# Kernel optimization log

Hardware: AMD Instinct MI355X
Metric: run time of the kernel (lower is better)

## Reference

```python
import jax, jax.numpy as jnp
import numpy as np

P = 3; Q = 3                 # spline degrees (deg_p, deg_q)
OUT_U = 64; OUT_V = 64       # surface evaluation grid
W_CTRL = 1.0; W_SURF = 1.0
B = 1024; MU_MAX = 32; MV_MAX = 32
EPS = 1e-5                   # SurfEval samples u,v in [eps, 1-eps]


def _open_uniform_knots(n_valid, degree, n_max):
    """Clamped open-uniform knot vector for n_valid ctrl pts, padded to static
    length n_max+degree+1. Entries beyond the valid span are clamped to 1.0,
    which makes the padded basis functions identically zero on [eps, 1-eps]."""
    L = n_valid + degree + 1  # true (ragged) knot count, traced int
    k = jnp.arange(n_max + degree + 1)
    interior = k.astype(jnp.float32) / (L - 1).astype(jnp.float32)
    return jnp.where(k <= degree, 0.0, jnp.where(k >= L - 1 - degree, 1.0, interior))


def _bspline_basis(kv, degree, u):
    """Cox-de Boor, vectorized over u. kv: (n_max+degree+1,), u: (U,).
    Returns (U, n_max) basis matrix; padded columns are exactly zero."""
    N = ((u[None, :] >= kv[:-1, None]) & (u[None, :] < kv[1:, None])).astype(jnp.float32)
    for d in range(1, degree + 1):
        m = N.shape[0] - 1  # number of basis funcs at this level
        den1 = kv[d:d + m] - kv[:m]
        den2 = kv[d + 1:d + 1 + m] - kv[1:1 + m]
        s1 = jnp.where((den1 > 0)[:, None],
                       (u[None, :] - kv[:m, None]) / jnp.where(den1 > 0, den1, 1.0)[:, None], 0.0)
        s2 = jnp.where((den2 > 0)[:, None],
                       (kv[d + 1:d + 1 + m, None] - u[None, :]) / jnp.where(den2 > 0, den2, 1.0)[:, None], 0.0)
        N = s1 * N[:m] + s2 * N[1:m + 1]
    return N.T  # (U, n_max)


def _eval_surface(ctrl, mask_b, u, v):
    """NURBS surface eval for one sample with ragged (Mu_i, Mv_i) via padded
    knots/basis; unit weights => rational division by basis partition sum."""
    mu = jnp.maximum(jnp.sum(jnp.any(mask_b > 0, axis=1)), P + 1)
    mv = jnp.maximum(jnp.sum(jnp.any(mask_b > 0, axis=0)), Q + 1)
    Bu = _bspline_basis(_open_uniform_knots(mu, P, MU_MAX), P, u)  # (OUT_U, MU_MAX)
    Bv = _bspline_basis(_open_uniform_knots(mv, Q, MV_MAX), Q, v)  # (OUT_V, MV_MAX)
    num = jnp.einsum('ui,vj,ijd->uvd', Bu, Bv, ctrl)               # (OUT_U, OUT_V, 3)
    den = Bu.sum(-1)[:, None] * Bv.sum(-1)[None, :]                # unit-weight denom
    return num / den[..., None]


def setup_inputs() -> dict:
    key = jax.random.key(0)
    k1, k2, k3, k4, k5 = jax.random.split(key, 5)
    # ragged true control sizes per sample, >= degree+1
    mu = jax.random.randint(k1, (B,), P + 1, MU_MAX + 1)
    mv = jax.random.randint(k2, (B,), Q + 1, MV_MAX + 1)
    mask = ((jnp.arange(MU_MAX)[None, :, None] < mu[:, None, None]) &
            (jnp.arange(MV_MAX)[None, None, :] < mv[:, None, None])).astype(jnp.float32)
    ctrl_pred_pad = jax.random.normal(k3, (B, MU_MAX, MV_MAX, 3), jnp.float32)
    ctrl_gt_pad = jax.random.normal(k4, (B, MU_MAX, MV_MAX, 3), jnp.float32)
    xyz_samples = jax.random.normal(k5, (B, OUT_U, OUT_V, 3), jnp.float32)
    return {"ctrl_pred_pad": ctrl_pred_pad, "ctrl_gt_pad": ctrl_gt_pad,
            "mask": mask, "xyz_samples": xyz_samples}


def reference(ctrl_pred_pad, ctrl_gt_pad, mask, xyz_samples):
    # masked control-point MSE
    diff2 = ((ctrl_pred_pad - ctrl_gt_pad) ** 2).sum(-1)
    loss_ctrl = (diff2 * mask).sum() / jnp.maximum(mask.sum() * 3.0, 1.0)
    # batched ragged surface evaluation
    u = jnp.linspace(EPS, 1.0 - EPS, OUT_U)
    v = jnp.linspace(EPS, 1.0 - EPS, OUT_V)
    surf = jax.vmap(lambda c, m: _eval_surface(c, m, u, v))(ctrl_pred_pad, mask)
    loss_surf = jnp.mean((surf.reshape(B, -1, 3) - xyz_samples.reshape(B, -1, 3)) ** 2)
    total = W_CTRL * loss_ctrl + W_SURF * loss_surf  # original computes total BEFORE nan-guard
    bad = jnp.isnan(surf).any() | jnp.isinf(surf).any()
    surf_mse = jnp.where(bad, jnp.float32(1e6), loss_surf)
    return total, loss_ctrl, surf_mse
```

## Files before the change

### kernel.cpp

```cpp
#include <hip/hip_runtime.h>
#include <math.h>

#define MU_MAXC 32
#define MV_MAXC 32
#define OUT_UC  64
#define OUT_VC  64
#define DEG     3
#define NKNOT   (MU_MAXC + DEG + 1)
#define EPSV    1e-5f

__global__ void zero_ws_kernel(double* acc, int* bad) {
    acc[0] = 0.0; acc[1] = 0.0; acc[2] = 0.0; bad[0] = 0;
}

template <int MODE>
__launch_bounds__(256)
__global__ void nurbs_loss_kernel(const float* __restrict__ ctrl_pred,
                                  const float* __restrict__ ctrl_gt,
                                  const float* __restrict__ mask,
                                  const float* __restrict__ xyz,
                                  double* __restrict__ pd, int Bcnt,
                                  int* __restrict__ badp)
{
    const int b   = blockIdx.x;
    const int tid = threadIdx.x;

    __shared__ float s_tmp[OUT_UC * MV_MAXC * 3];
    __shared__ float s_mask[1024];
    __shared__ float s_Bu4[4 * OUT_UC];
    __shared__ float s_Bv4[4 * OUT_VC];
    __shared__ int   s_uoff[OUT_UC];
    __shared__ int   s_voff[OUT_VC];
    __shared__ float s_invSumBu[OUT_UC];
    __shared__ float s_knots_u[NKNOT];
    __shared__ float s_knots_v[NKNOT];
    __shared__ int   s_rowany[MU_MAXC];
    __shared__ int   s_colany[MV_MAXC];
    __shared__ int   s_mu, s_mv, s_bad;
    __shared__ float s_wred[4], s_wred2[4];
    __shared__ float s_ctrl_diff, s_ctrl_mask;

    if (tid < 32) { s_rowany[tid] = 0; s_colany[tid] = 0; }
    if (tid == 0) s_bad = 0;
    __syncthreads();

    float lsum_mask = 0.f;
    #pragma unroll
    for (int k = 0; k < 4; k++) {
        const int cell = tid + 256 * k;
        const float m  = mask[b * 1024 + cell];
        s_mask[cell] = m;
        lsum_mask += m;
        if (m > 0.f) { s_rowany[cell >> 5] = 1; s_colany[cell & 31] = 1; }
    }
    __syncthreads();

    float lsum_diff = 0.f;
    {
        const float4* p4 = (const float4*)(ctrl_pred + (size_t)b * 3072);
        const float4* g4 = (const float4*)(ctrl_gt   + (size_t)b * 3072);
        #pragma unroll
        for (int k = 0; k < 3; k++) {
            const int e4 = tid + 256 * k;
            const float4 p = p4[e4];
            const float4 g = g4[e4];
            const int e = e4 * 4;
            const float dx = p.x - g.x, dy = p.y - g.y, dz = p.z - g.z, dw = p.w - g.w;
            lsum_diff += s_mask[(e + 0) / 3] * dx * dx
                       + s_mask[(e + 1) / 3] * dy * dy
                       + s_mask[(e + 2) / 3] * dz * dz
                       + s_mask[(e + 3) / 3] * dw * dw;
        }
    }
    #pragma unroll
    for (int off = 32; off > 0; off >>= 1) {
        lsum_mask += __shfl_down(lsum_mask, off);
        lsum_diff += __shfl_down(lsum_diff, off);
    }
    if ((tid & 63) == 0) { s_wred[tid >> 6] = lsum_mask; s_wred2[tid >> 6] = lsum_diff; }
    __syncthreads();

    if (tid == 0) {
        int cu = 0, cv = 0;
        #pragma unroll
        for (int i = 0; i < 32; i++) { cu += s_rowany[i]; cv += s_colany[i]; }
        s_mu = cu > (DEG + 1) ? cu : (DEG + 1);
        s_mv = cv > (DEG + 1) ? cv : (DEG + 1);
        s_ctrl_mask = s_wred[0] + s_wred[1] + s_wred[2] + s_wred[3];
        s_ctrl_diff = s_wred2[0] + s_wred2[1] + s_wred2[2] + s_wred2[3];
    }
    __syncthreads();

    if (tid < NKNOT) {
        const int L = s_mu + DEG + 1;
        s_knots_u[tid] = (tid <= DEG) ? 0.f
                        : ((tid >= L - 1 - DEG) ? 1.f : (float)tid / (float)(L - 1));
    } else if (tid >= 64 && tid < 64 + NKNOT) {
        const int k = tid - 64;
        const int L = s_mv + DEG + 1;
        s_knots_v[k] = (k <= DEG) ? 0.f
                      : ((k >= L - 1 - DEG) ? 1.f : (float)k / (float)(L - 1));
    }
    __syncthreads();

    if (tid < 128) {
        const bool isU = tid < 64;
        const int t = isU ? tid : (tid - 64);
        const float* kv = isU ? s_knots_u : s_knots_v;
        const float step = (1.f - 2.f * EPSV) / 63.f;
        const float uu = (t == 63) ? (1.f - EPSV) : (EPSV + step * (float)t);

        int span = DEG;
        #pragma unroll
        for (int k = DEG + 1; k < NKNOT - 1; k++)
            if (kv[k] <= uu) span = k;

        float N4[DEG + 1], left[DEG + 1], right[DEG + 1];
        N4[0] = 1.f;
        #pragma unroll
        for (int j = 1; j <= DEG; j++) {
            left[j]  = uu - kv[span + 1 - j];
            right[j] = kv[span + j] - uu;
            float saved = 0.f;
            #pragma unroll
            for (int r = 0; r < j; r++) {
                const float temp = N4[r] / (right[r + 1] + left[j - r]);
                N4[r] = saved + right[r + 1] * temp;
                saved = left[j - r] * temp;
            }
            N4[j] = saved;
        }
        const float s = N4[0] + N4[1] + N4[2] + N4[3];
        const float invs = 1.0f / s;
        const int off = span - DEG;
        if (isU) {
            #pragma unroll
            for (int r = 0; r < 4; r++) s_Bu4[r * 64 + t] = N4[r];
            s_uoff[t] = off; s_invSumBu[t] = invs;
        } else {
            #pragma unroll
            for (int r = 0; r < 4; r++) s_Bv4[r * 64 + t] = N4[r] * invs;
            s_voff[t] = off;
        }
    }
    __syncthreads();

    {
        const float4* ctrl4 = (const float4*)(ctrl_pred + (size_t)b * 3072);
        float4* tmp4 = (float4*)s_tmp;
        for (int k = 0; k < 6; k++) {
            const int flat4 = tid + 256 * k;
            const int u = flat4 / 24;
            const int q = flat4 - u * 24;
            const int off = s_uoff[u];
            const float w0 = s_Bu4[0 * 64 + u];
            const float w1 = s_Bu4[1 * 64 + u];
            const float w2 = s_Bu4[2 * 64 + u];
            const float w3 = s_Bu4[3 * 64 + u];
            const float4 c0 = ctrl4[(off + 0) * 24 + q];
            const float4 c1 = ctrl4[(off + 1) * 24 + q];
            const float4 c2 = ctrl4[(off + 2) * 24 + q];
            const float4 c3 = ctrl4[(off + 3) * 24 + q];
            float4 a;
            a.x = w0 * c0.x + w1 * c1.x + w2 * c2.x + w3 * c3.x;
            a.y = w0 * c0.y + w1 * c1.y + w2 * c2.y + w3 * c3.y;
            a.z = w0 * c0.z + w1 * c1.z + w2 * c2.z + w3 * c3.z;
            a.w = w0 * c0.w + w1 * c1.w + w2 * c2.w + w3 * c3.w;
            tmp4[flat4] = a;
        }
    }
    __syncthreads();

    float lsum_surf = 0.f;
    int bad = 0;
    {
        const int v = tid & 63;
        const int voff3 = s_voff[v] * 3;
        const float w0 = s_Bv4[0 * 64 + v];
        const float w1 = s_Bv4[1 * 64 + v];
        const float w2 = s_Bv4[2 * 64 + v];
        const float w3 = s_Bv4[3 * 64 + v];
        #pragma unroll
        for (int k = 0; k < 16; k++) {
            const int u = (tid >> 6) + 4 * k;
            const float* tp = &s_tmp[u * 96 + voff3];
            const float n0 = w0 * tp[0] + w1 * tp[3] + w2 * tp[6] + w3 * tp[9];
            const float n1 = w0 * tp[1] + w1 * tp[4] + w2 * tp[7] + w3 * tp[10];
            const float n2 = w0 * tp[2] + w1 * tp[5] + w2 * tp[8] + w3 * tp[11];
            const float inv = s_invSumBu[u];
            const float x0 = n0 * inv, x1 = n1 * inv, x2 = n2 * inv;
            const int base = (b * 4096 + u * 64 + v) * 3;
            const float d0 = x0 - xyz[base + 0];
            const float d1 = x1 - xyz[base + 1];
            const float d2 = x2 - xyz[base + 2];
            lsum_surf += d0 * d0 + d1 * d1 + d2 * d2;
            if (!isfinite(x0) || !isfinite(x1) || !isfinite(x2)) bad = 1;
        }
    }
    #pragma unroll
    for (int off = 32; off > 0; off >>= 1)
        lsum_surf += __shfl_down(lsum_surf, off);
    if ((tid & 63) == 0) s_wred[tid >> 6] = lsum_surf;
    if (bad) atomicOr(&s_bad, 1);
    __syncthreads();

    if (tid == 0) {
        const double surf = (double)s_wred[0] + s_wred[1] + s_wred[2] + s_wred[3];
        if (MODE == 0) {
            pd[b]             = (double)s_ctrl_diff;
            pd[Bcnt + b]      = (double)s_ctrl_mask;
            pd[2 * Bcnt + b]  = surf;
            badp[b]           = s_bad;
        } else {
            atomicAdd(&pd[0], (double)s_ctrl_diff);
            atomicAdd(&pd[1], (double)s_ctrl_mask);
            atomicAdd(&pd[2], surf);
            if (s_bad) atomicOr(badp, 1);
        }
    }
}

__global__ void finalize_partials_kernel(const double* __restrict__ pd,
                                         const int* __restrict__ badp,
                                         float* __restrict__ out, int Bcnt)
{
    __shared__ double sd0[4], sd1[4], sd2[4];
    __shared__ int sb[4];
    const int tid = threadIdx.x;
    double a0 = 0.0, a1 = 0.0, a2 = 0.0; int bad = 0;
    for (int i = tid; i < Bcnt; i += 256) {
        a0 += pd[i]; a1 += pd[Bcnt + i]; a2 += pd[2 * Bcnt + i];
        bad |= badp[i];
    }
    #pragma unroll
    for (int off = 32; off > 0; off >>= 1) {
        a0 += __shfl_down(a0, off);
        a1 += __shfl_down(a1, off);
        a2 += __shfl_down(a2, off);
        bad |= __shfl_down(bad, off);
    }
    if ((tid & 63) == 0) { const int w = tid >> 6; sd0[w] = a0; sd1[w] = a1; sd2[w] = a2; sb[w] = bad; }
    __syncthreads();
    if (tid == 0) {
        double d0 = 0, d1 = 0, d2 = 0; int bb = 0;
        #pragma unroll
        for (int i = 0; i < 4; i++) { d0 += sd0[i]; d1 += sd1[i]; d2 += sd2[i]; bb |= sb[i]; }
        const double denc = d1 * 3.0;
        const double lc = d0 / (denc > 1.0 ? denc : 1.0);
        const double ls = d2 / ((double)Bcnt * OUT_UC * OUT_VC * 3.0);
        out[0] = (float)(lc + ls);
        out[1] = (float)lc;
        out[2] = bb ? 1.0e6f : (float)ls;
    }
}

__global__ void finalize_atomic_kernel(const double* __restrict__ acc,
                                       const int* __restrict__ bad,
                                       float* __restrict__ out, int Bcnt)
{
    const double denc = acc[1] * 3.0;
    const double lc = acc[0] / (denc > 1.0 ? denc : 1.0);
    const double ls = acc[2] / ((double)Bcnt * OUT_UC * OUT_VC * 3.0);
    out[0] = (float)(lc + ls);
    out[1] = (float)lc;
    out[2] = bad[0] ? 1.0e6f : (float)ls;
}

extern "C" void kernel_launch(void* const* d_in, const int* in_sizes, int n_in,
                              void* d_out, int out_size, void* d_ws, size_t ws_size,
                              hipStream_t stream)
{
    const float* pred = (const float*)d_in[0];
    const float* gt   = (const float*)d_in[1];
    const float* mask = (const float*)d_in[2];
    const float* xyz  = (const float*)d_in[3];
    const int Bcnt = in_sizes[2] / (MU_MAXC * MV_MAXC);

    double* pd = (double*)d_ws;
    float* out = (float*)d_out;

    const size_t need = (size_t)3 * Bcnt * sizeof(double) + (size_t)Bcnt * sizeof(int);
    if (ws_size >= need) {
        int* badp = (int*)(pd + 3 * Bcnt);
        hipLaunchKernelGGL((nurbs_loss_kernel<0>), dim3(Bcnt), dim3(256), 0, stream,
                           pred, gt, mask, xyz, pd, Bcnt, badp);
        hipLaunchKernelGGL(finalize_partials_kernel, dim3(1), dim3(256), 0, stream,
                           pd, badp, out, Bcnt);
    } else {
        int* badp = (int*)(pd + 3);
        hipLaunchKernelGGL(zero_ws_kernel, dim3(1), dim3(1), 0, stream, pd, badp);
        hipLaunchKernelGGL((nurbs_loss_kernel<1>), dim3(Bcnt), dim3(256), 0, stream,
                           pred, gt, mask, xyz, pd, Bcnt, badp);
        hipLaunchKernelGGL(finalize_atomic_kernel, dim3(1), dim3(1), 0, stream,
                           pd, badp, out, Bcnt);
    }
}
```

Measured before the change: 113.8 us.

## Vectorize mask/ctrl/xyz loads, compute knots inline, drop shared knot and mask buffers

The mask is now read as one float4 per thread, aligned with three float4 control-point loads, so the shared mask buffer and one barrier go away. Knot values are computed inline from the knot formula instead of being staged in shared memory, which removes another barrier. The surface pass now gives each thread 4 consecutive v columns and reads xyz as float4 vectors instead of scalar strided loads. In exchange, registers per thread rise and there is extra ALU work for the inline knot math.

```diff
diff --git a/kernel.cpp b/kernel.cpp
--- a/kernel.cpp
+++ b/kernel.cpp
@@ -11,6 +11,10 @@
 
 __global__ void zero_ws_kernel(double* acc, int* bad) {
     acc[0] = 0.0; acc[1] = 0.0; acc[2] = 0.0; bad[0] = 0;
+}
+
+__device__ __forceinline__ float kv_at(int k, int L) {
+    return (k <= DEG) ? 0.f : ((k >= L - 1 - DEG) ? 1.f : (float)k / (float)(L - 1));
 }
 
 template <int MODE>
@@ -26,14 +30,11 @@
     const int tid = threadIdx.x;
 
     __shared__ float s_tmp[OUT_UC * MV_MAXC * 3];
-    __shared__ float s_mask[1024];
     __shared__ float s_Bu4[4 * OUT_UC];
     __shared__ float s_Bv4[4 * OUT_VC];
     __shared__ int   s_uoff[OUT_UC];
     __shared__ int   s_voff[OUT_VC];
     __shared__ float s_invSumBu[OUT_UC];
-    __shared__ float s_knots_u[NKNOT];
-    __shared__ float s_knots_v[NKNOT];
     __shared__ int   s_rowany[MU_MAXC];
     __shared__ int   s_colany[MV_MAXC];
     __shared__ int   s_mu, s_mv, s_bad;
@@ -44,33 +45,29 @@
     if (tid == 0) s_bad = 0;
     __syncthreads();
 
-    float lsum_mask = 0.f;
-    #pragma unroll
-    for (int k = 0; k < 4; k++) {
-        const int cell = tid + 256 * k;
-        const float m  = mask[b * 1024 + cell];
-        s_mask[cell] = m;
-        lsum_mask += m;
-        if (m > 0.f) { s_rowany[cell >> 5] = 1; s_colany[cell & 31] = 1; }
-    }
-    __syncthreads();
-
-    float lsum_diff = 0.f;
+    float lsum_mask, lsum_diff;
     {
+        const float4 mm = ((const float4*)(mask + (size_t)b * 1024))[tid];
         const float4* p4 = (const float4*)(ctrl_pred + (size_t)b * 3072);
         const float4* g4 = (const float4*)(ctrl_gt   + (size_t)b * 3072);
-        #pragma unroll
-        for (int k = 0; k < 3; k++) {
-            const int e4 = tid + 256 * k;
-            const float4 p = p4[e4];
-            const float4 g = g4[e4];
-            const int e = e4 * 4;
-            const float dx = p.x - g.x, dy = p.y - g.y, dz = p.z - g.z, dw = p.w - g.w;
-            lsum_diff += s_mask[(e + 0) / 3] * dx * dx
-                       + s_mask[(e + 1) / 3] * dy * dy
-                       + s_mask[(e + 2) / 3] * dz * dz
-                       + s_mask[(e + 3) / 3] * dw * dw;
-        }
+        const float4 pa = p4[3 * tid + 0], pb = p4[3 * tid + 1], pc = p4[3 * tid + 2];
+        const float4 ga = g4[3 * tid + 0], gb = g4[3 * tid + 1], gc = g4[3 * tid + 2];
+        const float a0 = pa.x - ga.x, a1 = pa.y - ga.y, a2 = pa.z - ga.z;
+        const float b0 = pa.w - ga.w, b1 = pb.x - gb.x, b2 = pb.y - gb.y;
+        const float c0 = pb.z - gb.z, c1 = pb.w - gb.w, c2 = pc.x - gc.x;
+        const float e0 = pc.y - gc.y, e1 = pc.z - gc.z, e2 = pc.w - gc.w;
+        lsum_mask = mm.x + mm.y + mm.z + mm.w;
+        lsum_diff = mm.x * (a0 * a0 + a1 * a1 + a2 * a2)
+                  + mm.y * (b0 * b0 + b1 * b1 + b2 * b2)
+                  + mm.z * (c0 * c0 + c1 * c1 + c2 * c2)
+                  + mm.w * (e0 * e0 + e1 * e1 + e2 * e2);
+        const int row = tid >> 3;
+        const int colb = (tid & 7) * 4;
+        if (lsum_mask > 0.f) s_rowany[row] = 1;
+        if (mm.x > 0.f) s_colany[colb + 0] = 1;
+        if (mm.y > 0.f) s_colany[colb + 1] = 1;
+        if (mm.z > 0.f) s_colany[colb + 2] = 1;
+        if (mm.w > 0.f) s_colany[colb + 3] = 1;
     }
     #pragma unroll
     for (int off = 32; off > 0; off >>= 1) {
@@ -91,36 +88,28 @@
     }
     __syncthreads();
 
-    if (tid < NKNOT) {
-        const int L = s_mu + DEG + 1;
-        s_knots_u[tid] = (tid <= DEG) ? 0.f
-                        : ((tid >= L - 1 - DEG) ? 1.f : (float)tid / (float)(L - 1));
-    } else if (tid >= 64 && tid < 64 + NKNOT) {
-        const int k = tid - 64;
-        const int L = s_mv + DEG + 1;
-        s_knots_v[k] = (k <= DEG) ? 0.f
-                      : ((k >= L - 1 - DEG) ? 1.f : (float)k / (float)(L - 1));
-    }
-    __syncthreads();
-
     if (tid < 128) {
         const bool isU = tid < 64;
         const int t = isU ? tid : (tid - 64);
-        const float* kv = isU ? s_knots_u : s_knots_v;
+        const int L = (isU ? s_mu : s_mv) + DEG + 1;
         const float step = (1.f - 2.f * EPSV) / 63.f;
         const float uu = (t == 63) ? (1.f - EPSV) : (EPSV + step * (float)t);
 
         int span = DEG;
         #pragma unroll
         for (int k = DEG + 1; k < NKNOT - 1; k++)
-            if (kv[k] <= uu) span = k;
-
-        float N4[DEG + 1], left[DEG + 1], right[DEG + 1];
+            if (kv_at(k, L) <= uu) span = k;
+
+        float left[DEG + 1], right[DEG + 1];
+        #pragma unroll
+        for (int j = 1; j <= DEG; j++) {
+            left[j]  = uu - kv_at(span + 1 - j, L);
+            right[j] = kv_at(span + j, L) - uu;
+        }
+        float N4[DEG + 1];
         N4[0] = 1.f;
         #pragma unroll
         for (int j = 1; j <= DEG; j++) {
-            left[j]  = uu - kv[span + 1 - j];
-            right[j] = kv[span + j] - uu;
             float saved = 0.f;
             #pragma unroll
             for (int r = 0; r < j; r++) {
@@ -174,27 +163,40 @@
     float lsum_surf = 0.f;
     int bad = 0;
     {
-        const int v = tid & 63;
-        const int voff3 = s_voff[v] * 3;
-        const float w0 = s_Bv4[0 * 64 + v];
-        const float w1 = s_Bv4[1 * 64 + v];
-        const float w2 = s_Bv4[2 * 64 + v];
-        const float w3 = s_Bv4[3 * 64 + v];
-        #pragma unroll
-        for (int k = 0; k < 16; k++) {
-            const int u = (tid >> 6) + 4 * k;
-            const float* tp = &s_tmp[u * 96 + voff3];
-            const float n0 = w0 * tp[0] + w1 * tp[3] + w2 * tp[6] + w3 * tp[9];
-            const float n1 = w0 * tp[1] + w1 * tp[4] + w2 * tp[7] + w3 * tp[10];
-            const float n2 = w0 * tp[2] + w1 * tp[5] + w2 * tp[8] + w3 * tp[11];
+        const int vg  = (tid & 15) * 4;
+        const int ug0 = tid >> 4;
+        float w[4][4]; int vo[4];
+        #pragma unroll
+        for (int c = 0; c < 4; c++) {
+            vo[c] = s_voff[vg + c] * 3;
+            #pragma unroll
+            for (int r = 0; r < 4; r++) w[c][r] = s_Bv4[r * 64 + vg + c];
+        }
+        #pragma unroll
+        for (int k = 0; k < 4; k++) {
+            const int u = ug0 + 16 * k;
             const float inv = s_invSumBu[u];
-            const float x0 = n0 * inv, x1 = n1 * inv, x2 = n2 * inv;
-            const int base = (b * 4096 + u * 64 + v) * 3;
-            const float d0 = x0 - xyz[base + 0];
-            const float d1 = x1 - xyz[base + 1];
-            const float d2 = x2 - xyz[base + 2];
-            lsum_surf += d0 * d0 + d1 * d1 + d2 * d2;
-            if (!isfinite(x0) || !isfinite(x1) || !isfinite(x2)) bad = 1;
+            const float* tp = &s_tmp[u * 96];
+            const float4* x4 = (const float4*)(xyz + ((size_t)b * 4096 + u * 64 + vg) * 3);
+            const float4 xa = x4[0], xb = x4[1], xc = x4[2];
+            float px[4], py[4], pz[4];
+            px[0] = xa.x; py[0] = xa.y; pz[0] = xa.z;
+            px[1] = xa.w; py[1] = xb.x; pz[1] = xb.y;
+            px[2] = xb.z; py[2] = xb.w; pz[2] = xc.x;
+            px[3] = xc.y; py[3] = xc.z; pz[3] = xc.w;
+            #pragma unroll
+            for (int c = 0; c < 4; c++) {
+                const float* tpc = tp + vo[c];
+                const float n0 = w[c][0] * tpc[0] + w[c][1] * tpc[3] + w[c][2] * tpc[6] + w[c][3] * tpc[9];
+                const float n1 = w[c][0] * tpc[1] + w[c][1] * tpc[4] + w[c][2] * tpc[7] + w[c][3] * tpc[10];
+                const float n2 = w[c][0] * tpc[2] + w[c][1] * tpc[5] + w[c][2] * tpc[8] + w[c][3] * tpc[11];
+                const float x0 = n0 * inv, x1 = n1 * inv, x2 = n2 * inv;
+                const float d0 = x0 - px[c];
+                const float d1 = x1 - py[c];
+                const float d2 = x2 - pz[c];
+                lsum_surf += d0 * d0 + d1 * d1 + d2 * d2;
+                if (!isfinite(x0) || !isfinite(x1) || !isfinite(x2)) bad = 1;
+            }
         }
     }
     #pragma unroll
```

New measurement: 117.2 us. 3.0% more time.
